# Performance work log

Measured on AMD Instinct MI355X. Metric: run time of the kernel, lower is better.

The kernel has to match this reference:

```python
import jax, jax.numpy as jnp
import numpy as np

B, N, D = 4096, 32768, 1024

def _l2norm(x, eps=1e-12):
    # matches F.normalize(p=2, dim=-1): x / max(||x||, eps)
    n = jnp.sqrt(jnp.sum(x * x, axis=-1, keepdims=True))
    return x / jnp.maximum(n, eps)

def setup_inputs() -> dict:
    key = jax.random.key(0)
    k1, k2, k3 = jax.random.split(key, 3)
    return {
        "query": jax.random.normal(k1, (B, D), dtype=jnp.float32),
        "keys": jax.random.normal(k2, (N, D), dtype=jnp.float32),
        "values": jax.random.normal(k3, (N, D), dtype=jnp.float32),
    }

def reference(query, keys, values):
    q = _l2norm(query.astype(jnp.float32))          # [B, D]
    k = _l2norm(keys.astype(jnp.float32))           # [N, D]
    v = values.astype(jnp.float32)                  # [N, Dv]
    sim = jnp.einsum('bd,nd->bn', q, k)             # [B, N] cosine similarities
    # torch .var(dim=-1) is unbiased (ddof=1)
    attention_var = jnp.var(sim, axis=-1, ddof=1).mean()
    best = jnp.argmax(sim, axis=-1)                 # [B]
    retrieved = v[best]                             # [B, Dv] gather
    return retrieved, attention_var
```

## Files before the change

kernel.cpp:

```cpp
#include <hip/hip_runtime.h>
#include <math.h>
#include <stdint.h>

#define B_ 4096
#define N_ 32768
#define D_ 1024

#define BM 128
#define BN 128
#define NT 2
#define NCHUNK 128
#define KTOT 32
#define QG (B_ / 16)
#define KG (N_ / 16)

typedef __attribute__((ext_vector_type(8))) short short8;
typedef __attribute__((ext_vector_type(4))) float f4;
typedef unsigned short u16;

__device__ __forceinline__ u16 bf16_rn(float x) {
    uint32_t u = __float_as_uint(x);
    u += 0x7fffu + ((u >> 16) & 1u);
    return (u16)(u >> 16);
}

__device__ __forceinline__ void split4(f4 v, uint2& hpack, uint2& lpack) {
    u16 h[4], l[4];
    #pragma unroll
    for (int e = 0; e < 4; ++e) {
        float x = v[e];
        u16 hb = bf16_rn(x);
        float hf = __uint_as_float(((uint32_t)hb) << 16);
        h[e] = hb;
        l[e] = bf16_rn(x - hf);
    }
    hpack.x = (uint32_t)h[0] | ((uint32_t)h[1] << 16);
    hpack.y = (uint32_t)h[2] | ((uint32_t)h[3] << 16);
    lpack.x = (uint32_t)l[0] | ((uint32_t)l[1] << 16);
    lpack.y = (uint32_t)l[2] | ((uint32_t)l[3] << 16);
}

__device__ __forceinline__ void g2l16(const void* g, void* l) {
    __builtin_amdgcn_global_load_lds(
        (const __attribute__((address_space(1))) char*)(uintptr_t)g,
        (__attribute__((address_space(3))) char*)(uint32_t)(uintptr_t)l,
        16, 0, 0);
}

__global__ __launch_bounds__(256) void pack_kernel(
    const float* __restrict__ q, const float* __restrict__ k,
    float* __restrict__ invq, float* __restrict__ invk,
    u16* __restrict__ qhi, u16* __restrict__ qlo,
    u16* __restrict__ khi, u16* __restrict__ klo,
    float* __restrict__ out)
{
    const int g = blockIdx.x;
    const int lane = threadIdx.x & 63;
    const int w = threadIdx.x >> 6;

    const float* src; float* invdst;
    u16 *dhi, *dlo; int groups, gg;
    if (g < B_ / 16) { src = q; invdst = invq; dhi = qhi; dlo = qlo; groups = QG; gg = g; }
    else { src = k; invdst = invk; dhi = khi; dlo = klo; groups = KG; gg = g - B_ / 16; }

    const int row = gg * 16 + (lane & 15);
    const int kofs = (lane >> 4) * 8;
    const float* rp = src + (size_t)row * D_;

    f4 v0[8], v1[8];
    float s = 0.f;
    #pragma unroll
    for (int u = 0; u < 8; ++u) {
        const int kt = w + u * 4;
        v0[u] = *(const f4*)(rp + kt * 32 + kofs);
        v1[u] = *(const f4*)(rp + kt * 32 + kofs + 4);
        #pragma unroll
        for (int e = 0; e < 4; ++e) {
            s = fmaf(v0[u][e], v0[u][e], s);
            s = fmaf(v1[u][e], v1[u][e], s);
        }
    }
    s += __shfl_xor(s, 16);
    s += __shfl_xor(s, 32);
    __shared__ float red[4][16];
    if ((lane >> 4) == 0) red[w][lane & 15] = s;
    __syncthreads();
    const float tot = red[0][lane & 15] + red[1][lane & 15]
                    + red[2][lane & 15] + red[3][lane & 15];
    const float scale = 1.0f / fmaxf(sqrtf(tot), 1e-12f);
    if (w == 0 && lane < 16) invdst[gg * 16 + lane] = scale;

    #pragma unroll
    for (int u = 0; u < 8; ++u) {
        const int kt = w + u * 4;
        f4 a = v0[u] * scale, b = v1[u] * scale;
        uint2 h0, l0, h1, l1;
        split4(a, h0, l0);
        split4(b, h1, l1);
        const size_t cbase = ((size_t)kt * groups + gg) * 512 + lane * 8;
        uint4 hh = {h0.x, h0.y, h1.x, h1.y};
        uint4 ll = {l0.x, l0.y, l1.x, l1.y};
        *(uint4*)(dhi + cbase) = hh;
        *(uint4*)(dlo + cbase) = ll;
    }
    if (g == 0 && threadIdx.x == 0) out[(size_t)B_ * D_] = 0.0f;
}

__global__ __launch_bounds__(256) void sim_stats_kernel(
    const u16* __restrict__ qhi, const u16* __restrict__ qlo,
    const u16* __restrict__ khi, const u16* __restrict__ klo,
    float* __restrict__ partials)
{
    __shared__ __align__(16) char smem[65536];

    const int tid = threadIdx.x;
    const int lane = tid & 63;
    const int w = tid >> 6;
    const int wm = w >> 1, wn = w & 1;
    const int quad = lane >> 4;
    const int l16 = lane & 15;
    const int mtile = blockIdx.x;
    const int chunk = blockIdx.y;
    const int b0 = mtile * BM;

    const u16* sbase = (w == 0) ? qhi : (w == 1) ? qlo : (w == 2) ? khi : klo;
    const int groups = (w < 2) ? (B_ / 16) : (N_ / 16);

    float (*scan)[68] = (float(*)[68])smem;

    float r_sum = 0.f, r_sq = 0.f, r_m1 = -INFINITY, r_m2 = -INFINITY;
    int r_i1 = 0x7fffffff, r_i2 = 0x7fffffff;

    const f4 zf = {0.f, 0.f, 0.f, 0.f};

    for (int nt = 0; nt < NT; ++nt) {
        const int n0 = chunk * (BN * NT) + nt * BN;
        const int g0 = ((w < 2) ? b0 : n0) >> 4;

        __syncthreads();
        {
            const size_t cb = ((size_t)0 * groups + g0) * 512 + lane * 8;
            char* dst = smem + w * 8192;
            #pragma unroll
            for (int t = 0; t < 8; ++t)
                g2l16(sbase + cb + t * 512, dst + t * 1024);
        }

        f4 acc[4][4];
        #pragma unroll
        for (int i = 0; i < 4; ++i)
            #pragma unroll
            for (int j = 0; j < 4; ++j) acc[i][j] = zf;

        for (int kt = 0; kt < KTOT; ++kt) {
            const int cur = kt & 1;
            __syncthreads();
            if (kt + 1 < KTOT) {
                const size_t cb = ((size_t)(kt + 1) * groups + g0) * 512 + lane * 8;
                char* dst = smem + (1 - cur) * 32768 + w * 8192;
                #pragma unroll
                for (int t = 0; t < 8; ++t)
                    g2l16(sbase + cb + t * 512, dst + t * 1024);
            }
            const char* cbuf = smem + cur * 32768;

            short8 ah[4], al[4];
            #pragma unroll
            for (int i = 0; i < 4; ++i) {
                ah[i] = *(const short8*)(cbuf + (wm * 4 + i) * 1024 + lane * 16);
                al[i] = *(const short8*)(cbuf + 8192 + (wm * 4 + i) * 1024 + lane * 16);
            }
            #pragma unroll
            for (int j = 0; j < 4; ++j) {
                short8 bh = *(const short8*)(cbuf + 16384 + (wn * 4 + j) * 1024 + lane * 16);
                short8 bl = *(const short8*)(cbuf + 24576 + (wn * 4 + j) * 1024 + lane * 16);
                #pragma unroll
                for (int i = 0; i < 4; ++i) {
                    acc[i][j] = __builtin_amdgcn_mfma_f32_16x16x32_bf16(ah[i], bh, acc[i][j], 0, 0, 0);
                    acc[i][j] = __builtin_amdgcn_mfma_f32_16x16x32_bf16(ah[i], bl, acc[i][j], 0, 0, 0);
                    acc[i][j] = __builtin_amdgcn_mfma_f32_16x16x32_bf16(al[i], bh, acc[i][j], 0, 0, 0);
                }
            }
        }

        const int srow = tid >> 1;
        const int c0 = (tid & 1) * 32;
        #pragma unroll 1
        for (int h = 0; h < 2; ++h) {
            __syncthreads();
            if (wn == h) {
                #pragma unroll
                for (int i = 0; i < 4; ++i)
                    #pragma unroll
                    for (int j = 0; j < 4; ++j)
                        #pragma unroll
                        for (int p = 0; p < 4; ++p)
                            scan[wm*64 + i*16 + quad*4 + p][j*16 + l16] = acc[i][j][p];
            }
            __syncthreads();
            const int gbase = n0 + h * 64 + c0;
            #pragma unroll
            for (int u = 0; u < 8; ++u) {
                const f4 v = *(const f4*)&scan[srow][c0 + 4*u];
                #pragma unroll
                for (int e = 0; e < 4; ++e) {
                    const float sv = v[e];
                    const int gi = gbase + 4*u + e;
                    r_sum += sv;
                    r_sq = fmaf(sv, sv, r_sq);
                    if (sv > r_m1)      { r_m2 = r_m1; r_i2 = r_i1; r_m1 = sv; r_i1 = gi; }
                    else if (sv > r_m2) { r_m2 = sv; r_i2 = gi; }
                }
            }
        }
    }

    __syncthreads();
    float* mb = (float*)smem;
    mb[tid*6+0] = r_sum; mb[tid*6+1] = r_sq;
    mb[tid*6+2] = r_m1;  mb[tid*6+3] = __int_as_float(r_i1);
    mb[tid*6+4] = r_m2;  mb[tid*6+5] = __int_as_float(r_i2);
    __syncthreads();
    if ((tid & 1) == 0) {
        const float* o = mb + (size_t)(tid + 1) * 6;
        const float bs = o[0], bq = o[1], bm1 = o[2], bm2 = o[4];
        const int bi1 = __float_as_int(o[3]), bi2 = __float_as_int(o[5]);
        float s = r_sum + bs, q2 = r_sq + bq;
        float m1 = r_m1, m2 = r_m2; int i1 = r_i1, i2 = r_i2;
        if (bm1 > m1 || (bm1 == m1 && bi1 < i1)) {
            float nm2; int ni2;
            if (m1 > bm2 || (m1 == bm2 && i1 < bi2)) { nm2 = m1; ni2 = i1; }
            else                                     { nm2 = bm2; ni2 = bi2; }
            m1 = bm1; i1 = bi1; m2 = nm2; i2 = ni2;
        } else if (bm1 > m2 || (bm1 == m2 && bi1 < i2)) {
            m2 = bm1; i2 = bi1;
        }
        const int row = b0 + (tid >> 1);
        float* p = partials + ((size_t)row * NCHUNK + chunk) * 8;
        f4 p0 = {s, q2, m1, __int_as_float(i1)};
        f4 p1 = {m2, __int_as_float(i2), 0.f, 0.f};
        *(f4*)p = p0;
        *(f4*)(p + 4) = p1;
    }
}

__global__ __launch_bounds__(64) void finalize_kernel(
    const float* __restrict__ partials,
    const float* __restrict__ qg, const float* __restrict__ kg,
    const float* __restrict__ values,
    const float* __restrict__ invq, const float* __restrict__ invk,
    float* __restrict__ out)
{
    const int b = blockIdx.x;
    const int lane = threadIdx.x;

    float s = 0.f, q2 = 0.f, m1 = -INFINITY, m2 = -INFINITY;
    int i1 = 0x7fffffff, i2 = 0x7fffffff;
    #pragma unroll
    for (int cc = 0; cc < NCHUNK / 64; ++cc) {
        const int c = lane + cc * 64;
        const float* p = partials + ((size_t)b * NCHUNK + c) * 8;
        const float bs = p[0], bq = p[1], bm1 = p[2], bm2 = p[4];
        const int bi1 = __float_as_int(p[3]), bi2 = __float_as_int(p[5]);
        s += bs; q2 += bq;
        if (bm1 > m1 || (bm1 == m1 && bi1 < i1)) {
            float nm2; int ni2;
            if (m1 > bm2 || (m1 == bm2 && i1 < bi2)) { nm2 = m1; ni2 = i1; }
            else                                     { nm2 = bm2; ni2 = bi2; }
            m1 = bm1; i1 = bi1; m2 = nm2; i2 = ni2;
        } else if (bm1 > m2 || (bm1 == m2 && bi1 < i2)) {
            m2 = bm1; i2 = bi1;
        }
    }
    #pragma unroll
    for (int msk = 1; msk < 64; msk <<= 1) {
        const float bs = __shfl_xor(s, msk), bq = __shfl_xor(q2, msk);
        const float bm1 = __shfl_xor(m1, msk), bm2 = __shfl_xor(m2, msk);
        const int bi1 = __shfl_xor(i1, msk), bi2 = __shfl_xor(i2, msk);
        s += bs; q2 += bq;
        if (bm1 > m1 || (bm1 == m1 && bi1 < i1)) {
            float nm2; int ni2;
            if (m1 > bm2 || (m1 == bm2 && i1 < bi2)) { nm2 = m1; ni2 = i1; }
            else                                     { nm2 = bm2; ni2 = bi2; }
            m1 = bm1; i1 = bi1; m2 = nm2; i2 = ni2;
        } else if (bm1 > m2 || (bm1 == m2 && bi1 < i2)) {
            m2 = bm1; i2 = bi1;
        }
    }
    if (lane == 0) {
        const float var = (q2 - s * s / (float)N_) / (float)(N_ - 1);
        atomicAdd(out + (size_t)B_ * D_, var * (1.0f / B_));
    }

    const float* qrow = qg + (size_t)b * D_;
    const float* k1 = kg + (size_t)i1 * D_;
    const float* k2 = kg + (size_t)i2 * D_;
    double d1 = 0.0, d2 = 0.0;
    #pragma unroll
    for (int v4 = 0; v4 < 4; ++v4) {
        const int off = v4 * 256 + lane * 4;
        const f4 qv = *(const f4*)(qrow + off);
        const f4 a1 = *(const f4*)(k1 + off);
        const f4 a2 = *(const f4*)(k2 + off);
        #pragma unroll
        for (int e = 0; e < 4; ++e) {
            d1 += (double)qv[e] * (double)a1[e];
            d2 += (double)qv[e] * (double)a2[e];
        }
    }
    #pragma unroll
    for (int msk = 1; msk < 64; msk <<= 1) {
        d1 += __shfl_xor(d1, msk);
        d2 += __shfl_xor(d2, msk);
    }
    const double sc = (double)invq[b];
    const double s1 = d1 * sc * (double)invk[i1];
    const double s2 = d2 * sc * (double)invk[i2];
    const int winner = (s2 > s1 || (s2 == s1 && i2 < i1)) ? i2 : i1;

    const float* vrow = values + (size_t)winner * D_;
    float* orow = out + (size_t)b * D_;
    #pragma unroll
    for (int v4 = 0; v4 < 4; ++v4) {
        const int off = v4 * 256 + lane * 4;
        *(f4*)(orow + off) = *(const f4*)(vrow + off);
    }
}

extern "C" void kernel_launch(void* const* d_in, const int* in_sizes, int n_in,
                              void* d_out, int out_size, void* d_ws, size_t ws_size,
                              hipStream_t stream)
{
    const float* q = (const float*)d_in[0];
    const float* k = (const float*)d_in[1];
    const float* v = (const float*)d_in[2];
    float* out = (float*)d_out;
    float* ws = (float*)d_ws;

    float* invq = ws;
    float* invk = ws + B_;
    float* partials = ws + B_ + N_;
    u16* qhi = (u16*)(partials + (size_t)B_ * NCHUNK * 8);
    u16* qlo = qhi + (size_t)B_ * D_;
    u16* khi = qlo + (size_t)B_ * D_;
    u16* klo = khi + (size_t)N_ * D_;

    pack_kernel<<<(B_ + N_) / 16, 256, 0, stream>>>(q, k, invq, invk, qhi, qlo, khi, klo, out);
    sim_stats_kernel<<<dim3(B_ / BM, NCHUNK), 256, 0, stream>>>(qhi, qlo, khi, klo, partials);
    finalize_kernel<<<B_, 64, 0, stream>>>(partials, q, k, v, invq, invk, out);
}
```

Measured before the change: 980.2 us.

## Switch split-bf16 GEMM from 16x16x32 to 32x32x16 MFMA with repacked layout

Replaces the 16x16x32 bf16 MFMA tiles with 32x32x16 MFMA tiles, so each wave holds 2x2 accumulators of 16 floats instead of 4x4 of 4. The pack kernel now writes Q and K in 32-row groups with 16-wide k slices to match the larger instruction's operand layout. The sim kernel's staging loads and the accumulator scatter into LDS are updated to the new fragment mapping. The aim is to issue fewer MFMA instructions and fewer LDS fragment reads per k-step. The cost is a more intricate index mapping that must match the instruction's output layout exactly.

```diff
diff --git a/kernel.cpp b/kernel.cpp
--- a/kernel.cpp
+++ b/kernel.cpp
@@ -11,11 +11,12 @@
 #define NT 2
 #define NCHUNK 128
 #define KTOT 32
-#define QG (B_ / 16)
-#define KG (N_ / 16)
+#define QG32 (B_ / 32)
+#define KG32 (N_ / 32)
 
 typedef __attribute__((ext_vector_type(8))) short short8;
 typedef __attribute__((ext_vector_type(4))) float f4;
+typedef __attribute__((ext_vector_type(16))) float f16v;
 typedef unsigned short u16;
 
 __device__ __forceinline__ u16 bf16_rn(float x) {
@@ -59,13 +60,15 @@
     const int w = threadIdx.x >> 6;
 
     const float* src; float* invdst;
-    u16 *dhi, *dlo; int groups, gg;
-    if (g < B_ / 16) { src = q; invdst = invq; dhi = qhi; dlo = qlo; groups = QG; gg = g; }
-    else { src = k; invdst = invk; dhi = khi; dlo = klo; groups = KG; gg = g - B_ / 16; }
-
-    const int row = gg * 16 + (lane & 15);
+    u16 *dhi, *dlo; int groups32, gg;
+    if (g < B_ / 16) { src = q; invdst = invq; dhi = qhi; dlo = qlo; groups32 = QG32; gg = g; }
+    else { src = k; invdst = invk; dhi = khi; dlo = klo; groups32 = KG32; gg = g - B_ / 16; }
+
+    const int row_local = gg * 16 + (lane & 15);
+    const int g32 = row_local >> 5;
+    const int r32 = row_local & 31;
     const int kofs = (lane >> 4) * 8;
-    const float* rp = src + (size_t)row * D_;
+    const float* rp = src + (size_t)row_local * D_;
 
     f4 v0[8], v1[8];
     float s = 0.f;
@@ -90,14 +93,16 @@
     const float scale = 1.0f / fmaxf(sqrtf(tot), 1e-12f);
     if (w == 0 && lane < 16) invdst[gg * 16 + lane] = scale;
 
+    const int k8 = (kofs >> 3) & 1;
     #pragma unroll
     for (int u = 0; u < 8; ++u) {
         const int kt = w + u * 4;
+        const int kt16 = kt * 2 + (kofs >> 4);
         f4 a = v0[u] * scale, b = v1[u] * scale;
         uint2 h0, l0, h1, l1;
         split4(a, h0, l0);
         split4(b, h1, l1);
-        const size_t cbase = ((size_t)kt * groups + gg) * 512 + lane * 8;
+        const size_t cbase = ((size_t)kt16 * groups32 + g32) * 512 + (r32 + 32 * k8) * 8;
         uint4 hh = {h0.x, h0.y, h1.x, h1.y};
         uint4 ll = {l0.x, l0.y, l1.x, l1.y};
         *(uint4*)(dhi + cbase) = hh;
@@ -117,69 +122,75 @@
     const int lane = tid & 63;
     const int w = tid >> 6;
     const int wm = w >> 1, wn = w & 1;
-    const int quad = lane >> 4;
-    const int l16 = lane & 15;
+    const int l32 = lane & 31;
+    const int lhi = lane >> 5;
     const int mtile = blockIdx.x;
     const int chunk = blockIdx.y;
     const int b0 = mtile * BM;
 
     const u16* sbase = (w == 0) ? qhi : (w == 1) ? qlo : (w == 2) ? khi : klo;
-    const int groups = (w < 2) ? (B_ / 16) : (N_ / 16);
+    const int groups = (w < 2) ? QG32 : KG32;
 
     float (*scan)[68] = (float(*)[68])smem;
 
     float r_sum = 0.f, r_sq = 0.f, r_m1 = -INFINITY, r_m2 = -INFINITY;
     int r_i1 = 0x7fffffff, r_i2 = 0x7fffffff;
 
-    const f4 zf = {0.f, 0.f, 0.f, 0.f};
-
     for (int nt = 0; nt < NT; ++nt) {
         const int n0 = chunk * (BN * NT) + nt * BN;
-        const int g0 = ((w < 2) ? b0 : n0) >> 4;
+        const int g0 = ((w < 2) ? b0 : n0) >> 5;
 
         __syncthreads();
         {
-            const size_t cb = ((size_t)0 * groups + g0) * 512 + lane * 8;
             char* dst = smem + w * 8192;
             #pragma unroll
-            for (int t = 0; t < 8; ++t)
-                g2l16(sbase + cb + t * 512, dst + t * 1024);
-        }
-
-        f4 acc[4][4];
+            for (int t = 0; t < 8; ++t) {
+                const int h = t >> 2, gi = t & 3;
+                const size_t cb = ((size_t)h * groups + g0 + gi) * 512 + lane * 8;
+                g2l16(sbase + cb, dst + t * 1024);
+            }
+        }
+
+        f16v acc[2][2];
         #pragma unroll
-        for (int i = 0; i < 4; ++i)
+        for (int i = 0; i < 2; ++i)
             #pragma unroll
-            for (int j = 0; j < 4; ++j) acc[i][j] = zf;
+            for (int j = 0; j < 2; ++j)
+                #pragma unroll
+                for (int p = 0; p < 16; ++p) acc[i][j][p] = 0.f;
 
         for (int kt = 0; kt < KTOT; ++kt) {
             const int cur = kt & 1;
             __syncthreads();
             if (kt + 1 < KTOT) {
-                const size_t cb = ((size_t)(kt + 1) * groups + g0) * 512 + lane * 8;
                 char* dst = smem + (1 - cur) * 32768 + w * 8192;
                 #pragma unroll
-                for (int t = 0; t < 8; ++t)
-                    g2l16(sbase + cb + t * 512, dst + t * 1024);
+                for (int t = 0; t < 8; ++t) {
+                    const int h = t >> 2, gi = t & 3;
+                    const size_t cb = ((size_t)((kt + 1) * 2 + h) * groups + g0 + gi) * 512 + lane * 8;
+                    g2l16(sbase + cb, dst + t * 1024);
+                }
             }
             const char* cbuf = smem + cur * 32768;
 
-            short8 ah[4], al[4];
             #pragma unroll
-            for (int i = 0; i < 4; ++i) {
-                ah[i] = *(const short8*)(cbuf + (wm * 4 + i) * 1024 + lane * 16);
-                al[i] = *(const short8*)(cbuf + 8192 + (wm * 4 + i) * 1024 + lane * 16);
-            }
-            #pragma unroll
-            for (int j = 0; j < 4; ++j) {
-                short8 bh = *(const short8*)(cbuf + 16384 + (wn * 4 + j) * 1024 + lane * 16);
-                short8 bl = *(const short8*)(cbuf + 24576 + (wn * 4 + j) * 1024 + lane * 16);
-                #pragma unroll
-                for (int i = 0; i < 4; ++i) {
-                    acc[i][j] = __builtin_amdgcn_mfma_f32_16x16x32_bf16(ah[i], bh, acc[i][j], 0, 0, 0);
-                    acc[i][j] = __builtin_amdgcn_mfma_f32_16x16x32_bf16(ah[i], bl, acc[i][j], 0, 0, 0);
-                    acc[i][j] = __builtin_amdgcn_mfma_f32_16x16x32_bf16(al[i], bh, acc[i][j], 0, 0, 0);
+            for (int h = 0; h < 2; ++h) {
+                short8 ah[2], al[2], bh[2], bl[2];
+                #pragma unroll
+                for (int i = 0; i < 2; ++i) {
+                    ah[i] = *(const short8*)(cbuf + (h * 4 + wm * 2 + i) * 1024 + lane * 16);
+                    al[i] = *(const short8*)(cbuf + 8192 + (h * 4 + wm * 2 + i) * 1024 + lane * 16);
+                    bh[i] = *(const short8*)(cbuf + 16384 + (h * 4 + wn * 2 + i) * 1024 + lane * 16);
+                    bl[i] = *(const short8*)(cbuf + 24576 + (h * 4 + wn * 2 + i) * 1024 + lane * 16);
                 }
+                #pragma unroll
+                for (int j = 0; j < 2; ++j)
+                    #pragma unroll
+                    for (int i = 0; i < 2; ++i) {
+                        acc[i][j] = __builtin_amdgcn_mfma_f32_32x32x16_bf16(ah[i], bh[j], acc[i][j], 0, 0, 0);
+                        acc[i][j] = __builtin_amdgcn_mfma_f32_32x32x16_bf16(ah[i], bl[j], acc[i][j], 0, 0, 0);
+                        acc[i][j] = __builtin_amdgcn_mfma_f32_32x32x16_bf16(al[i], bh[j], acc[i][j], 0, 0, 0);
+                    }
             }
         }
 
@@ -190,12 +201,12 @@
             __syncthreads();
             if (wn == h) {
                 #pragma unroll
-                for (int i = 0; i < 4; ++i)
+                for (int i = 0; i < 2; ++i)
                     #pragma unroll
-                    for (int j = 0; j < 4; ++j)
+                    for (int j = 0; j < 2; ++j)
                         #pragma unroll
-                        for (int p = 0; p < 4; ++p)
-                            scan[wm*64 + i*16 + quad*4 + p][j*16 + l16] = acc[i][j][p];
+                        for (int p = 0; p < 16; ++p)
+                            scan[wm*64 + i*32 + ((p & 3) + 8*(p >> 2) + 4*lhi)][j*32 + l32] = acc[i][j][p];
             }
             __syncthreads();
             const int gbase = n0 + h * 64 + c0;
```

Result: slower. 1.093 ms (+11.5%).

## Load query-lo tile directly from global to cut LDS and raise occupancy

Applied to the files above, without the earlier changes.

The qlo operand is no longer staged through shared memory. Each wave now loads its own query low-part fragments straight from global memory, so the LDS double buffer shrinks from 64KB to 48KB. The launch bound is raised to 3 blocks per CU to exploit the freed LDS, and staging work is redistributed as 6 chunks per wave. The MFMA order is changed so the al*bh products run after the hi products. The cost is extra global-memory latency on the al loads and tighter register pressure from the occupancy hint.

```diff
diff --git a/kernel.cpp b/kernel.cpp
--- a/kernel.cpp
+++ b/kernel.cpp
@@ -106,12 +106,12 @@
     if (g == 0 && threadIdx.x == 0) out[(size_t)B_ * D_] = 0.0f;
 }
 
-__global__ __launch_bounds__(256) void sim_stats_kernel(
+__global__ __launch_bounds__(256, 3) void sim_stats_kernel(
     const u16* __restrict__ qhi, const u16* __restrict__ qlo,
     const u16* __restrict__ khi, const u16* __restrict__ klo,
     float* __restrict__ partials)
 {
-    __shared__ __align__(16) char smem[65536];
+    __shared__ __align__(16) char smem[49152];
 
     const int tid = threadIdx.x;
     const int lane = tid & 63;
@@ -123,8 +123,8 @@
     const int chunk = blockIdx.y;
     const int b0 = mtile * BM;
 
-    const u16* sbase = (w == 0) ? qhi : (w == 1) ? qlo : (w == 2) ? khi : klo;
-    const int groups = (w < 2) ? (B_ / 16) : (N_ / 16);
+    const int aG0 = b0 >> 4;
+    const int aG0w = aG0 + wm * 4;
 
     float (*scan)[68] = (float(*)[68])smem;
 
@@ -135,16 +135,25 @@
 
     for (int nt = 0; nt < NT; ++nt) {
         const int n0 = chunk * (BN * NT) + nt * BN;
-        const int g0 = ((w < 2) ? b0 : n0) >> 4;
+        const int bG0 = n0 >> 4;
+
+        auto stage = [&](int kt, char* dstbase) {
+            #pragma unroll
+            for (int t = 0; t < 6; ++t) {
+                const int c = w * 6 + t;
+                const bool isA  = (c < 8);
+                const bool isBh = (c >= 8) && (c < 16);
+                const u16* sp = isA ? qhi : (isBh ? khi : klo);
+                const int idx = isA ? c : (isBh ? (c - 8) : (c - 16));
+                const int gg  = (isA ? aG0 : bG0) + idx;
+                const int grp = isA ? QG : KG;
+                const size_t cb = ((size_t)kt * grp + gg) * 512 + lane * 8;
+                g2l16(sp + cb, dstbase + c * 1024);
+            }
+        };
 
         __syncthreads();
-        {
-            const size_t cb = ((size_t)0 * groups + g0) * 512 + lane * 8;
-            char* dst = smem + w * 8192;
-            #pragma unroll
-            for (int t = 0; t < 8; ++t)
-                g2l16(sbase + cb + t * 512, dst + t * 1024);
-        }
+        stage(0, smem);
 
         f4 acc[4][4];
         #pragma unroll
@@ -155,32 +164,39 @@
         for (int kt = 0; kt < KTOT; ++kt) {
             const int cur = kt & 1;
             __syncthreads();
-            if (kt + 1 < KTOT) {
-                const size_t cb = ((size_t)(kt + 1) * groups + g0) * 512 + lane * 8;
-                char* dst = smem + (1 - cur) * 32768 + w * 8192;
-                #pragma unroll
-                for (int t = 0; t < 8; ++t)
-                    g2l16(sbase + cb + t * 512, dst + t * 1024);
-            }
-            const char* cbuf = smem + cur * 32768;
-
-            short8 ah[4], al[4];
-            #pragma unroll
-            for (int i = 0; i < 4; ++i) {
+
+            short8 al[4];
+            {
+                const size_t ab = ((size_t)kt * QG + aG0w) * 512 + lane * 8;
+                #pragma unroll
+                for (int i = 0; i < 4; ++i)
+                    al[i] = *(const short8*)(qlo + ab + i * 512);
+            }
+
+            if (kt + 1 < KTOT)
+                stage(kt + 1, smem + (1 - cur) * 24576);
+
+            const char* cbuf = smem + cur * 24576;
+
+            short8 ah[4], bhk[4];
+            #pragma unroll
+            for (int i = 0; i < 4; ++i)
                 ah[i] = *(const short8*)(cbuf + (wm * 4 + i) * 1024 + lane * 16);
-                al[i] = *(const short8*)(cbuf + 8192 + (wm * 4 + i) * 1024 + lane * 16);
-            }
             #pragma unroll
             for (int j = 0; j < 4; ++j) {
-                short8 bh = *(const short8*)(cbuf + 16384 + (wn * 4 + j) * 1024 + lane * 16);
-                short8 bl = *(const short8*)(cbuf + 24576 + (wn * 4 + j) * 1024 + lane * 16);
+                bhk[j] = *(const short8*)(cbuf + 8192 + (wn * 4 + j) * 1024 + lane * 16);
+                short8 bl = *(const short8*)(cbuf + 16384 + (wn * 4 + j) * 1024 + lane * 16);
                 #pragma unroll
                 for (int i = 0; i < 4; ++i) {
-                    acc[i][j] = __builtin_amdgcn_mfma_f32_16x16x32_bf16(ah[i], bh, acc[i][j], 0, 0, 0);
+                    acc[i][j] = __builtin_amdgcn_mfma_f32_16x16x32_bf16(ah[i], bhk[j], acc[i][j], 0, 0, 0);
                     acc[i][j] = __builtin_amdgcn_mfma_f32_16x16x32_bf16(ah[i], bl, acc[i][j], 0, 0, 0);
-                    acc[i][j] = __builtin_amdgcn_mfma_f32_16x16x32_bf16(al[i], bh, acc[i][j], 0, 0, 0);
                 }
             }
+            #pragma unroll
+            for (int j = 0; j < 4; ++j)
+                #pragma unroll
+                for (int i = 0; i < 4; ++i)
+                    acc[i][j] = __builtin_amdgcn_mfma_f32_16x16x32_bf16(al[i], bhk[j], acc[i][j], 0, 0, 0);
         }
 
         const int srow = tid >> 1;
```

New measurement: 1.753 ms. 1.79x slower.
